# Performance work log

Measured on AMD Instinct MI355X. Metric: run time of the kernel, lower is better.

Reference implementation:

```python
import jax, jax.numpy as jnp
import numpy as np

BATCH = 2048
SEQ_LEN = 8192


def setup_inputs() -> dict:
    key = jax.random.key(0)
    k1, k2 = jax.random.split(key)
    inputs = jax.random.normal(k1, (BATCH, SEQ_LEN), dtype=jnp.float32)
    filters = jax.random.normal(k2, (BATCH, SEQ_LEN), dtype=jnp.float32)
    return {"inputs": inputs, "filters": filters}


def reference(inputs, filters):
    # FFT-based long convolution with zero-padding to 2L (linear, not circular, conv).
    # torch norm='forward': rfft divides by n, irfft multiplies by n -> net scale 1/n.
    L = inputs.shape[-1]
    n = 2 * L  # rfft with n=2L implicitly zero-pads, same as F.pad then rfft
    x_f = jnp.fft.rfft(inputs, n=n, axis=-1, norm="forward")   # (B, L+1) complex
    h_f = jnp.fft.rfft(filters, n=n, axis=-1, norm="forward")  # (B, L+1) complex
    y = jnp.fft.irfft(x_f * h_f, n=n, axis=-1, norm="forward")  # (B, 2L)
    return y[..., :L]
```

## Files before the change

### kernel.cpp

```cpp
#include <hip/hip_runtime.h>

#define L_LEN 8192
#define N_FFT 16384
#define NB    1024

#define LB __launch_bounds__(NB)

typedef float f2 __attribute__((ext_vector_type(2)));

__device__ __forceinline__ f2 mkf2(float a, float b) { f2 v; v.x = a; v.y = b; return v; }

__device__ __forceinline__ f2 cmul(f2 a, f2 w) {
    return mkf2(a.y, a.y) * mkf2(-w.y, w.x) + mkf2(a.x, a.x) * w;
}

__host__ __device__ constexpr int swz(int i) {
    return i ^ ((((i) >> 4) ^ ((i) >> 8) ^ ((i) >> 12)) & 15);
}

__device__ __forceinline__ int rev4_12(int m) {
    int r = 0;
#pragma unroll
    for (int d = 0; d < 6; ++d) { r = (r << 2) | (m & 3); m >>= 2; }
    return r;
}

__device__ __forceinline__ void bfly_dif(f2& x0, f2& x1, f2& x2, f2& x3,
                                         f2 w1, f2 w2, f2 w3) {
    f2 A = x0 + x2, B = x0 - x2, C = x1 + x3, D = x1 - x3;
    f2 iD = mkf2(-D.y, D.x);
    x0 = A + C;
    x1 = cmul(B - iD, w1);
    x2 = cmul(A - C, w2);
    x3 = cmul(B + iD, w3);
}

__device__ __forceinline__ void bfly_dit(f2& x0, f2& x1, f2& x2, f2& x3,
                                         f2 w1, f2 w2, f2 w3) {
    f2 a1 = cmul(x1, w1), a2 = cmul(x2, w2), a3 = cmul(x3, w3);
    f2 E = x0 + a2, F = x0 - a2, G = a1 + a3, K = a1 - a3;
    f2 iK = mkf2(-K.y, K.x);
    x0 = E + G; x1 = F + iK; x2 = E - G; x3 = F - iK;
}

__device__ __forceinline__ void bfly_dif1(f2* z) {
    f2 A = z[0] + z[2], B = z[0] - z[2], C = z[1] + z[3], D = z[1] - z[3];
    f2 iD = mkf2(-D.y, D.x);
    z[0] = A + C; z[1] = B - iD; z[2] = A - C; z[3] = B + iD;
}
__device__ __forceinline__ void bfly_dit1(f2* z) {
    f2 E = z[0] + z[2], F = z[0] - z[2], G = z[1] + z[3], K = z[1] - z[3];
    f2 iK = mkf2(-K.y, K.x);
    z[0] = E + G; z[1] = F + iK; z[2] = E - G; z[3] = F - iK;
}

__device__ __forceinline__ void pointwise_pair(f2& Zm, f2& Zr) {
    f2 half = mkf2(0.5f, 0.5f);
    f2 X = half * (Zm + mkf2(Zr.x, -Zr.y));
    f2 H = half * (mkf2(Zm.y, -Zm.x) + mkf2(Zr.y, Zr.x));
    f2 Y = cmul(X, H);
    Zm = Y;
    Zr = mkf2(Y.x, -Y.y);
}

#define CT0 1.0f
#define CT1 0.92387953251128674f
#define CT2 0.70710678118654752f
#define CT3 0.38268343236508977f
#define ST1 0.38268343236508977f
#define ST2 0.70710678118654752f
#define ST3 0.92387953251128674f

template<int QA>
__device__ __forceinline__ void fwd_pair(f2* lds, int tid) {
    constexpr int QB = QA / 4;
    const int g = tid / QB;
    const int u = tid % QB;
    const int sb = swz(g * (4 * QA) + u);
    f2 r[4][4];
#pragma unroll
    for (int jA = 0; jA < 4; ++jA)
#pragma unroll
        for (int jB = 0; jB < 4; ++jB)
            r[jA][jB] = lds[sb ^ swz(jA * QA + jB * QB)];

    {
        const float angA = -6.283185307179586f / (float)(4 * QA);
        float sn, cs;
        __sincosf(angA * (float)u, &sn, &cs);
        f2 u1 = mkf2(cs, sn);
        const f2 lad[4] = {mkf2(CT0, 0.f), mkf2(CT1, -ST1), mkf2(CT2, -ST2), mkf2(CT3, -ST3)};
#pragma unroll
        for (int jB = 0; jB < 4; ++jB) {
            f2 w1 = (jB == 0) ? u1 : cmul(u1, lad[jB]);
            f2 w2 = cmul(w1, w1);
            f2 w3 = cmul(w2, w1);
            bfly_dif(r[0][jB], r[1][jB], r[2][jB], r[3][jB], w1, w2, w3);
        }
    }
    {
        const float angB = -6.283185307179586f / (float)(4 * QB);
        float sn, cs;
        __sincosf(angB * (float)u, &sn, &cs);
        f2 v1 = mkf2(cs, sn);
        f2 v2 = cmul(v1, v1);
        f2 v3 = cmul(v2, v1);
#pragma unroll
        for (int jA = 0; jA < 4; ++jA)
            bfly_dif(r[jA][0], r[jA][1], r[jA][2], r[jA][3], v1, v2, v3);
    }

#pragma unroll
    for (int jA = 0; jA < 4; ++jA)
#pragma unroll
        for (int jB = 0; jB < 4; ++jB)
            lds[sb ^ swz(jA * QA + jB * QB)] = r[jA][jB];
}

template<int QA>
__device__ __forceinline__ void inv_pair(f2* lds, int tid) {
    constexpr int QB = 4 * QA;
    const int G = tid / QA;
    const int u = tid % QA;
    const int sb = swz(G * (16 * QA) + u);
    f2 r[4][4];
#pragma unroll
    for (int jA = 0; jA < 4; ++jA)
#pragma unroll
        for (int jB = 0; jB < 4; ++jB)
            r[jA][jB] = lds[sb ^ swz(jA * QA + jB * QB)];

    {
        const float angA = 6.283185307179586f / (float)(4 * QA);
        float sn, cs;
        __sincosf(angA * (float)u, &sn, &cs);
        f2 a1 = mkf2(cs, sn);
        f2 a2 = cmul(a1, a1);
        f2 a3 = cmul(a2, a1);
#pragma unroll
        for (int jB = 0; jB < 4; ++jB)
            bfly_dit(r[0][jB], r[1][jB], r[2][jB], r[3][jB], a1, a2, a3);
    }
    {
        const float angB = 6.283185307179586f / (float)(4 * QB);
        float sn, cs;
        __sincosf(angB * (float)u, &sn, &cs);
        f2 b1 = mkf2(cs, sn);
        const f2 lad[4] = {mkf2(CT0, 0.f), mkf2(CT1, ST1), mkf2(CT2, ST2), mkf2(CT3, ST3)};
#pragma unroll
        for (int jA = 0; jA < 4; ++jA) {
            f2 w1 = (jA == 0) ? b1 : cmul(b1, lad[jA]);
            f2 w2 = cmul(w1, w1);
            f2 w3 = cmul(w2, w1);
            bfly_dit(r[jA][0], r[jA][1], r[jA][2], r[jA][3], w1, w2, w3);
        }
    }

#pragma unroll
    for (int jA = 0; jA < 4; ++jA)
#pragma unroll
        for (int jB = 0; jB < 4; ++jB)
            lds[sb ^ swz(jA * QA + jB * QB)] = r[jA][jB];
}

__global__ LB
void fftconv_kernel(const float* __restrict__ xin,
                    const float* __restrict__ hin,
                    float* __restrict__ out)
{
    __shared__ f2 lds[N_FFT];

    const int row = blockIdx.x;
    const int tid = threadIdx.x;
    const float* xr = xin + (size_t)row * L_LEN;
    const float* hr = hin + (size_t)row * L_LEN;

    const int s4t = swz(4 * tid);
#pragma unroll
    for (int iter = 0; iter < 2; ++iter) {
        float4 xv = ((const float4*)xr)[tid + iter * NB];
        float4 hv = ((const float4*)hr)[tid + iter * NB];
        lds[s4t ^ swz(iter * 4096 + 0)] = mkf2(xv.x, hv.x);
        lds[s4t ^ swz(iter * 4096 + 1)] = mkf2(xv.y, hv.y);
        lds[s4t ^ swz(iter * 4096 + 2)] = mkf2(xv.z, hv.z);
        lds[s4t ^ swz(iter * 4096 + 3)] = mkf2(xv.w, hv.w);
    }
    const int st = swz(tid);
#pragma unroll
    for (int it = 0; it < 8; ++it)
        lds[st ^ swz(8192 + it * 1024)] = mkf2(0.f, 0.f);
    __syncthreads();

    fwd_pair<4096>(lds, tid); __syncthreads();
    fwd_pair<256>(lds, tid);  __syncthreads();
    fwd_pair<16>(lds, tid);   __syncthreads();

#pragma unroll
    for (int iter = 0; iter < 2; ++iter) {
        const int p = tid + iter * NB;
        if (p == 0) {
            f2 z[4];
#pragma unroll
            for (int k = 0; k < 4; ++k) z[k] = lds[k];
            bfly_dif1(z);
            z[0] = mkf2(z[0].x * z[0].y, 0.f);
            z[2] = mkf2(z[2].x * z[2].y, 0.f);
            pointwise_pair(z[1], z[3]);
            bfly_dit1(z);
#pragma unroll
            for (int k = 0; k < 4; ++k) lds[k] = z[k];
            f2 w[4];
#pragma unroll
            for (int k = 0; k < 4; ++k) w[k] = lds[8 + k];
            bfly_dif1(w);
            pointwise_pair(w[0], w[3]);
            pointwise_pair(w[1], w[2]);
            bfly_dit1(w);
#pragma unroll
            for (int k = 0; k < 4; ++k) lds[8 + k] = w[k];
        } else {
            const int sA = swz(4 * rev4_12(p));
            const int sB = swz(4 * rev4_12(4096 - p));
            f2 A[4], B[4];
#pragma unroll
            for (int k = 0; k < 4; ++k) A[k] = lds[sA ^ k];
#pragma unroll
            for (int k = 0; k < 4; ++k) B[k] = lds[sB ^ k];
            bfly_dif1(A);
            bfly_dif1(B);
            pointwise_pair(A[0], B[3]);
            pointwise_pair(A[1], B[2]);
            pointwise_pair(A[2], B[1]);
            pointwise_pair(A[3], B[0]);
            bfly_dit1(A);
            bfly_dit1(B);
#pragma unroll
            for (int k = 0; k < 4; ++k) lds[sA ^ k] = A[k];
#pragma unroll
            for (int k = 0; k < 4; ++k) lds[sB ^ k] = B[k];
        }
    }
    __syncthreads();

    inv_pair<4>(lds, tid);    __syncthreads();
    inv_pair<64>(lds, tid);   __syncthreads();
    inv_pair<1024>(lds, tid); __syncthreads();

    const float scale = 1.0f / ((float)N_FFT * (float)N_FFT);
    float* orow = out + (size_t)row * L_LEN;
#pragma unroll
    for (int iter = 0; iter < 2; ++iter) {
        float4 o;
        o.x = lds[s4t ^ swz(iter * 4096 + 0)].x * scale;
        o.y = lds[s4t ^ swz(iter * 4096 + 1)].x * scale;
        o.z = lds[s4t ^ swz(iter * 4096 + 2)].x * scale;
        o.w = lds[s4t ^ swz(iter * 4096 + 3)].x * scale;
        ((float4*)orow)[tid + iter * NB] = o;
    }
}

extern "C" void kernel_launch(void* const* d_in, const int* in_sizes, int n_in,
                              void* d_out, int out_size, void* d_ws, size_t ws_size,
                              hipStream_t stream) {
    const float* x = (const float*)d_in[0];
    const float* h = (const float*)d_in[1];
    float* out = (float*)d_out;
    const int rows = in_sizes[0] / L_LEN;
    fftconv_kernel<<<dim3(rows), dim3(NB), 0, stream>>>(x, h, out);
}
```

Baseline: 126.6 us.

## Fuse global load into first FFT stage and final stage into output store

The first forward radix-16 pass now reads x and h straight from global memory and skips the zero half of the padded input. This removes the LDS staging writes, the explicit zero-fill and one barrier. The last inverse pass computes only the real outputs for the first L samples and writes them straight to global, dropping an LDS round trip and a barrier. In exchange, global loads become scalar strided-by-thread accesses (still coalesced across threads) instead of float4, and the output stores are scalar.

New measurement: 113.1 us. 10.7% less time.

```diff
diff --git a/kernel.cpp b/kernel.cpp
--- a/kernel.cpp
+++ b/kernel.cpp
@@ -71,6 +71,90 @@
 #define ST2 0.70710678118654752f
 #define ST3 0.92387953251128674f
 
+__device__ __forceinline__ void fwd_first(f2* lds, int tid,
+                                          const float* __restrict__ xr,
+                                          const float* __restrict__ hr) {
+    f2 r[4][4];
+    const float angA = -6.283185307179586f / 16384.f;
+    float snA, csA;
+    __sincosf(angA * (float)tid, &snA, &csA);
+    f2 u1 = mkf2(csA, snA);
+    const f2 lad[4] = {mkf2(CT0, 0.f), mkf2(CT1, -ST1), mkf2(CT2, -ST2), mkf2(CT3, -ST3)};
+#pragma unroll
+    for (int jB = 0; jB < 4; ++jB) {
+        const int t = tid + jB * 1024;
+        f2 z0 = mkf2(xr[t], hr[t]);
+        f2 z1 = mkf2(xr[t + 4096], hr[t + 4096]);
+        f2 w1 = (jB == 0) ? u1 : cmul(u1, lad[jB]);
+        f2 w2 = cmul(w1, w1);
+        f2 w3 = cmul(w2, w1);
+        f2 iz1 = mkf2(-z1.y, z1.x);
+        r[0][jB] = z0 + z1;
+        r[1][jB] = cmul(z0 - iz1, w1);
+        r[2][jB] = cmul(z0 - z1, w2);
+        r[3][jB] = cmul(z0 + iz1, w3);
+    }
+    const float angB = -6.283185307179586f / 4096.f;
+    float sn, cs;
+    __sincosf(angB * (float)tid, &sn, &cs);
+    f2 v1 = mkf2(cs, sn);
+    f2 v2 = cmul(v1, v1);
+    f2 v3 = cmul(v2, v1);
+#pragma unroll
+    for (int jA = 0; jA < 4; ++jA)
+        bfly_dif(r[jA][0], r[jA][1], r[jA][2], r[jA][3], v1, v2, v3);
+
+    const int sb = swz(tid);
+#pragma unroll
+    for (int jA = 0; jA < 4; ++jA)
+#pragma unroll
+        for (int jB = 0; jB < 4; ++jB)
+            lds[sb ^ swz(jA * 4096 + jB * 1024)] = r[jA][jB];
+}
+
+__device__ __forceinline__ void inv_last(const f2* lds, int tid,
+                                         float* __restrict__ orow) {
+    const int sb = swz(tid);
+    f2 r[4][4];
+#pragma unroll
+    for (int jA = 0; jA < 4; ++jA)
+#pragma unroll
+        for (int jB = 0; jB < 4; ++jB)
+            r[jA][jB] = lds[sb ^ swz(jA * 1024 + jB * 4096)];
+
+    {
+        const float angA = 6.283185307179586f / 4096.f;
+        float sn, cs;
+        __sincosf(angA * (float)tid, &sn, &cs);
+        f2 a1 = mkf2(cs, sn);
+        f2 a2 = cmul(a1, a1);
+        f2 a3 = cmul(a2, a1);
+#pragma unroll
+        for (int jB = 0; jB < 4; ++jB)
+            bfly_dit(r[0][jB], r[1][jB], r[2][jB], r[3][jB], a1, a2, a3);
+    }
+    const float scale = 1.0f / ((float)N_FFT * (float)N_FFT);
+    const float angB = 6.283185307179586f / 16384.f;
+    float sn, cs;
+    __sincosf(angB * (float)tid, &sn, &cs);
+    f2 b1 = mkf2(cs, sn);
+    const f2 lad[4] = {mkf2(CT0, 0.f), mkf2(CT1, ST1), mkf2(CT2, ST2), mkf2(CT3, ST3)};
+#pragma unroll
+    for (int jA = 0; jA < 4; ++jA) {
+        f2 w1 = (jA == 0) ? b1 : cmul(b1, lad[jA]);
+        f2 w2 = cmul(w1, w1);
+        f2 w3 = cmul(w2, w1);
+        f2 x0 = r[jA][0];
+        f2 a1 = cmul(r[jA][1], w1);
+        f2 a2 = cmul(r[jA][2], w2);
+        f2 a3 = cmul(r[jA][3], w3);
+        float y0 = x0.x + a2.x + a1.x + a3.x;
+        float y1 = x0.x - a2.x - a1.y + a3.y;
+        orow[tid + jA * 1024]        = y0 * scale;
+        orow[tid + jA * 1024 + 4096] = y1 * scale;
+    }
+}
+
 template<int QA>
 __device__ __forceinline__ void fwd_pair(f2* lds, int tid) {
     constexpr int QB = QA / 4;
@@ -175,25 +259,9 @@
     const float* xr = xin + (size_t)row * L_LEN;
     const float* hr = hin + (size_t)row * L_LEN;
 
-    const int s4t = swz(4 * tid);
-#pragma unroll
-    for (int iter = 0; iter < 2; ++iter) {
-        float4 xv = ((const float4*)xr)[tid + iter * NB];
-        float4 hv = ((const float4*)hr)[tid + iter * NB];
-        lds[s4t ^ swz(iter * 4096 + 0)] = mkf2(xv.x, hv.x);
-        lds[s4t ^ swz(iter * 4096 + 1)] = mkf2(xv.y, hv.y);
-        lds[s4t ^ swz(iter * 4096 + 2)] = mkf2(xv.z, hv.z);
-        lds[s4t ^ swz(iter * 4096 + 3)] = mkf2(xv.w, hv.w);
-    }
-    const int st = swz(tid);
-#pragma unroll
-    for (int it = 0; it < 8; ++it)
-        lds[st ^ swz(8192 + it * 1024)] = mkf2(0.f, 0.f);
-    __syncthreads();
-
-    fwd_pair<4096>(lds, tid); __syncthreads();
-    fwd_pair<256>(lds, tid);  __syncthreads();
-    fwd_pair<16>(lds, tid);   __syncthreads();
+    fwd_first(lds, tid, xr, hr); __syncthreads();
+    fwd_pair<256>(lds, tid);     __syncthreads();
+    fwd_pair<16>(lds, tid);      __syncthreads();
 
 #pragma unroll
     for (int iter = 0; iter < 2; ++iter) {
@@ -242,21 +310,9 @@
     }
     __syncthreads();
 
-    inv_pair<4>(lds, tid);    __syncthreads();
-    inv_pair<64>(lds, tid);   __syncthreads();
-    inv_pair<1024>(lds, tid); __syncthreads();
-
-    const float scale = 1.0f / ((float)N_FFT * (float)N_FFT);
-    float* orow = out + (size_t)row * L_LEN;
-#pragma unroll
-    for (int iter = 0; iter < 2; ++iter) {
-        float4 o;
-        o.x = lds[s4t ^ swz(iter * 4096 + 0)].x * scale;
-        o.y = lds[s4t ^ swz(iter * 4096 + 1)].x * scale;
-        o.z = lds[s4t ^ swz(iter * 4096 + 2)].x * scale;
-        o.w = lds[s4t ^ swz(iter * 4096 + 3)].x * scale;
-        ((float4*)orow)[tid + iter * NB] = o;
-    }
+    inv_pair<4>(lds, tid);  __syncthreads();
+    inv_pair<64>(lds, tid); __syncthreads();
+    inv_last(lds, tid, out + (size_t)row * L_LEN);
 }
 
 extern "C" void kernel_launch(void* const* d_in, const int* in_sizes, int n_in,
```
